# Performance work log

Measured on AMD Instinct MI355X. Metric: run time of the kernel, lower is better.

## Reference

```python
import jax, jax.numpy as jnp
import numpy as np

D_MODEL = 768
N_HEADS = 12
HEAD_DIM = D_MODEL // N_HEADS
B, T = 2, 2048


def setup_inputs() -> dict:
    key = jax.random.key(0)
    k1, k2, k3 = jax.random.split(key, 3)
    x = jax.random.normal(k1, (B, T, D_MODEL), dtype=jnp.float32)
    # causal mask: positions where mask == 0 (False) get -inf
    mask = jnp.tril(jnp.ones((T, T), dtype=bool))[None, None, :, :]
    Wqkv = jax.random.normal(k2, (D_MODEL, 3 * D_MODEL), dtype=jnp.float32) * (D_MODEL ** -0.5)
    bqkv = jnp.zeros((3 * D_MODEL,), dtype=jnp.float32)
    Wout = jax.random.normal(k3, (D_MODEL, D_MODEL), dtype=jnp.float32) * (D_MODEL ** -0.5)
    bout = jnp.zeros((D_MODEL,), dtype=jnp.float32)
    return {"x": x, "mask": mask, "Wqkv": Wqkv, "bqkv": bqkv, "Wout": Wout, "bout": bout}


def reference(x, mask, Wqkv, bqkv, Wout, bout):
    b, t, c = x.shape
    qkv = x @ Wqkv + bqkv                      # [B, T, 3C]
    q, k, v = jnp.split(qkv, 3, axis=-1)
    def heads(z):  # [B, T, C] -> [B, H, T, Dh]
        return z.reshape(b, t, N_HEADS, HEAD_DIM).transpose(0, 2, 1, 3)
    q, k, v = heads(q), heads(k), heads(v)
    scores = jnp.einsum('bhqd,bhkd->bhqk', q, k) / jnp.sqrt(jnp.float32(HEAD_DIM))
    scores = jnp.where(mask, scores, -jnp.inf)
    attn = jax.nn.softmax(scores, axis=-1)
    out = jnp.einsum('bhqk,bhkd->bhqd', attn, v)  # [B, H, T, Dh]
    out = out.transpose(0, 2, 1, 3).reshape(b, t, c)
    # dropout is identity in eval mode
    return out @ Wout + bout
```

## Files before the change

kernel.cpp:

```cpp
#include <hip/hip_runtime.h>
#include <math.h>

#define BB 2
#define TT 2048
#define CC 768
#define HH 12
#define DD 64
#define MROWS (BB*TT)
#define NQKV (3*CC)
#define QBLK 64

typedef short bf16x8 __attribute__((ext_vector_type(8)));
typedef float f32x4 __attribute__((ext_vector_type(4)));

__device__ __forceinline__ unsigned short f2bf(float f) {
    union { float f; unsigned u; } v; v.f = f;
    unsigned u = v.u + 0x7FFF + ((v.u >> 16) & 1);
    return (unsigned short)(u >> 16);
}

__device__ __forceinline__ unsigned cvtpk_bf16(float lo, float hi) {
    unsigned r;
    asm("v_cvt_pk_bf16_f32 %0, %1, %2" : "=v"(r) : "v"(lo), "v"(hi));
    return r;
}

__device__ __forceinline__ void gload_lds16(const void* g, void* l) {
    __builtin_amdgcn_global_load_lds(
        (const __attribute__((address_space(1))) unsigned int*)g,
        (__attribute__((address_space(3))) unsigned int*)l, 16, 0, 0);
}

#define XBLOCKS 512
#define TQKV_TILES ((NQKV/64)*(CC/64))
#define TOUT_TILES ((CC/64)*(CC/64))

__global__ __launch_bounds__(256) void prep(const float* __restrict__ x,
                                            const float* __restrict__ Wqkv,
                                            const float* __restrict__ Wout,
                                            unsigned short* __restrict__ xb,
                                            unsigned short* __restrict__ wqkv_t,
                                            unsigned short* __restrict__ wout_t)
{
    int bid = blockIdx.x;
    if (bid < XBLOCKS) {
        const int total8 = MROWS * CC / 8;
        for (int i = bid * 256 + threadIdx.x; i < total8; i += XBLOCKS * 256) {
            float4 a = ((const float4*)x)[i * 2];
            float4 b = ((const float4*)x)[i * 2 + 1];
            ushort4 lo = { f2bf(a.x), f2bf(a.y), f2bf(a.z), f2bf(a.w) };
            ushort4 hi = { f2bf(b.x), f2bf(b.y), f2bf(b.z), f2bf(b.w) };
            ((ushort4*)xb)[i * 2]     = lo;
            ((ushort4*)xb)[i * 2 + 1] = hi;
        }
        return;
    }
    bid -= XBLOCKS;
    const float* src; unsigned short* dst; int srcN, nt, kt;
    if (bid < TQKV_TILES) { src = Wqkv; dst = wqkv_t; srcN = NQKV;
                            nt = bid % (NQKV/64); kt = bid / (NQKV/64); }
    else { bid -= TQKV_TILES; src = Wout; dst = wout_t; srcN = CC;
           nt = bid % (CC/64); kt = bid / (CC/64); }

    __shared__ float Ts[64][65];
    const int n0 = nt * 64, k0 = kt * 64;
#pragma unroll
    for (int p = 0; p < 4; ++p) {
        int c = p * 256 + threadIdx.x;
        int row = c >> 4, col4 = c & 15;
        float4 v = *(const float4*)&src[(size_t)(k0 + row) * srcN + n0 + col4 * 4];
        Ts[row][col4 * 4 + 0] = v.x;
        Ts[row][col4 * 4 + 1] = v.y;
        Ts[row][col4 * 4 + 2] = v.z;
        Ts[row][col4 * 4 + 3] = v.w;
    }
    __syncthreads();
#pragma unroll
    for (int p = 0; p < 4; ++p) {
        int t = p * 256 + threadIdx.x;
        int on = t >> 4, oslot = t & 15;
        ushort4 o = { f2bf(Ts[oslot * 4 + 0][on]), f2bf(Ts[oslot * 4 + 1][on]),
                      f2bf(Ts[oslot * 4 + 2][on]), f2bf(Ts[oslot * 4 + 3][on]) };
        *(ushort4*)&dst[(size_t)(n0 + on) * CC + k0 + oslot * 4] = o;
    }
}

__global__ __launch_bounds__(256) void qkv_mfma(const unsigned short* __restrict__ A,
                                                const unsigned short* __restrict__ Bt,
                                                const float* __restrict__ bias,
                                                unsigned short* __restrict__ qb,
                                                unsigned short* __restrict__ kb,
                                                unsigned short* __restrict__ vb)
{
    __shared__ unsigned short As[64 * 64];
    __shared__ unsigned short Bs[128 * 64];
    const int tid = threadIdx.x;
    const int wv = tid >> 6, l = tid & 63, g = l >> 4, lr = l & 15;
    const int wm = wv >> 1, wn = wv & 1;
    const int m0 = blockIdx.y * 64, n0 = blockIdx.x * 128;
    const int h7 = lr & 7;

    f32x4 acc[2][4] = {};

    for (int k0 = 0; k0 < CC; k0 += 64) {
        __syncthreads();
#pragma unroll
        for (int p = 0; p < 2; ++p) {
            int c = p * 256 + tid;
            int row = c >> 3, slot = c & 7;
            int ss = slot ^ (row & 7);
            gload_lds16(A + (size_t)(m0 + row) * CC + k0 + ss * 8, As + c * 8);
        }
#pragma unroll
        for (int p = 0; p < 4; ++p) {
            int c = p * 256 + tid;
            int row = c >> 3, slot = c & 7;
            int ss = slot ^ (row & 7);
            gload_lds16(Bt + (size_t)(n0 + row) * CC + k0 + ss * 8, Bs + c * 8);
        }
        __syncthreads();
        bf16x8 af[2][2], bfr[4][2];
#pragma unroll
        for (int i = 0; i < 2; ++i)
#pragma unroll
            for (int kt = 0; kt < 2; ++kt) {
                int row = wm * 32 + i * 16 + lr;
                af[i][kt] = *(const bf16x8*)&As[row * 64 + ((kt * 4 + g) ^ h7) * 8];
            }
#pragma unroll
        for (int j = 0; j < 4; ++j)
#pragma unroll
            for (int kt = 0; kt < 2; ++kt) {
                int row = wn * 64 + j * 16 + lr;
                bfr[j][kt] = *(const bf16x8*)&Bs[row * 64 + ((kt * 4 + g) ^ h7) * 8];
            }
#pragma unroll
        for (int i = 0; i < 2; ++i)
#pragma unroll
            for (int j = 0; j < 4; ++j)
#pragma unroll
                for (int kt = 0; kt < 2; ++kt)
                    acc[i][j] = __builtin_amdgcn_mfma_f32_16x16x32_bf16(af[i][kt], bfr[j][kt], acc[i][j], 0, 0, 0);
    }

#pragma unroll
    for (int i = 0; i < 2; ++i)
#pragma unroll
        for (int r = 0; r < 4; ++r) {
            int m = m0 + wm * 32 + i * 16 + 4 * g + r;
            int b_ = m >> 11, t = m & (TT - 1);
#pragma unroll
            for (int j = 0; j < 4; ++j) {
                int n = n0 + wn * 64 + j * 16 + lr;
                float val = acc[i][j][r] + bias[n];
                int which = n / CC;
                int rr = n - which * CC;
                int h = rr >> 6, d = rr & 63;
                size_t bh = (size_t)b_ * HH + h;
                if (which == 0)      qb[(bh * TT + t) * DD + d] = f2bf(val * 0.18033688f);
                else if (which == 1) kb[(bh * TT + t) * DD + d] = f2bf(val);
                else                 vb[(bh * DD + d) * TT + t] = f2bf(val);
            }
        }
}

__global__ __launch_bounds__(256) void out_mfma(const unsigned short* __restrict__ A,
                                                const unsigned short* __restrict__ Bt,
                                                const float* __restrict__ bias,
                                                float* __restrict__ out)
{
    __shared__ unsigned short As[64 * 64];
    __shared__ unsigned short Bs[128 * 64];
    const int tid = threadIdx.x;
    const int wv = tid >> 6, l = tid & 63, g = l >> 4, lr = l & 15;
    const int wm = wv >> 1, wn = wv & 1;
    const int m0 = blockIdx.y * 64, n0 = blockIdx.x * 128;
    const int h7 = lr & 7;

    f32x4 acc[2][4] = {};

    for (int k0 = 0; k0 < CC; k0 += 64) {
        __syncthreads();
#pragma unroll
        for (int p = 0; p < 2; ++p) {
            int c = p * 256 + tid;
            int row = c >> 3, slot = c & 7;
            int ss = slot ^ (row & 7);
            gload_lds16(A + (size_t)(m0 + row) * CC + k0 + ss * 8, As + c * 8);
        }
#pragma unroll
        for (int p = 0; p < 4; ++p) {
            int c = p * 256 + tid;
            int row = c >> 3, slot = c & 7;
            int ss = slot ^ (row & 7);
            gload_lds16(Bt + (size_t)(n0 + row) * CC + k0 + ss * 8, Bs + c * 8);
        }
        __syncthreads();
        bf16x8 af[2][2], bfr[4][2];
#pragma unroll
        for (int i = 0; i < 2; ++i)
#pragma unroll
            for (int kt = 0; kt < 2; ++kt) {
                int row = wm * 32 + i * 16 + lr;
                af[i][kt] = *(const bf16x8*)&As[row * 64 + ((kt * 4 + g) ^ h7) * 8];
            }
#pragma unroll
        for (int j = 0; j < 4; ++j)
#pragma unroll
            for (int kt = 0; kt < 2; ++kt) {
                int row = wn * 64 + j * 16 + lr;
                bfr[j][kt] = *(const bf16x8*)&Bs[row * 64 + ((kt * 4 + g) ^ h7) * 8];
            }
#pragma unroll
        for (int i = 0; i < 2; ++i)
#pragma unroll
            for (int j = 0; j < 4; ++j)
#pragma unroll
                for (int kt = 0; kt < 2; ++kt)
                    acc[i][j] = __builtin_amdgcn_mfma_f32_16x16x32_bf16(af[i][kt], bfr[j][kt], acc[i][j], 0, 0, 0);
    }

#pragma unroll
    for (int i = 0; i < 2; ++i)
#pragma unroll
        for (int r = 0; r < 4; ++r) {
            int m = m0 + wm * 32 + i * 16 + 4 * g + r;
#pragma unroll
            for (int j = 0; j < 4; ++j) {
                int n = n0 + wn * 64 + j * 16 + lr;
                out[(size_t)m * CC + n] = acc[i][j][r] + bias[n];
            }
        }
}

__global__ __launch_bounds__(256) void attn_mfma(
    const unsigned short* __restrict__ qb,
    const unsigned short* __restrict__ kb,
    const unsigned short* __restrict__ vtb,
    unsigned short* __restrict__ outp)
{
    __shared__ unsigned short Ks[2 * 64 * 64];
    __shared__ unsigned short Vts[2 * 64 * 64];

    const int blk  = blockIdx.x;
    const int head = blk % (BB * HH);
    const int qt   = (TT / QBLK - 1) - blk / (BB * HH);
    const int tid  = threadIdx.x;
    const int wv   = tid >> 6;
    const int l    = tid & 63;
    const int g    = l >> 4;
    const int lr   = l & 15;

    const size_t hb = (size_t)head * TT * DD;
    const int qrow0 = qt * QBLK + wv * 16;

    bf16x8 qf[2];
#pragma unroll
    for (int dt = 0; dt < 2; ++dt)
        qf[dt] = *(const bf16x8*)(qb + hb + (size_t)(qrow0 + lr) * DD + dt * 32 + 8 * g);

    f32x4 oacc[4] = {};
    float lpart = 0.f;

    const int srow0 = tid >> 3, srow1 = srow0 + 32;
    const int slot  = tid & 7;
#define RHO(k) ((((k) >> 5) << 5) | ((((k) >> 2) & 1) << 4) | ((((k) >> 3) & 3) << 2) | ((k) & 3))
    const int rho0 = RHO(srow0), rho1 = RHO(srow1);
    const int koff0 = (rho0 * 64 + slot * 8) ^ ((rho0 & 7) << 3);
    const int koff1 = (rho1 * 64 + slot * 8) ^ ((rho1 & 7) << 3);
    const int voff0 = (srow0 * 64 + slot * 8) ^ ((srow0 & 7) << 3);
    const int voff1 = (srow1 * 64 + slot * 8) ^ ((srow1 & 7) << 3);
    const unsigned short* kg0 = kb  + hb + (size_t)srow0 * DD + slot * 8;
    const unsigned short* kg1 = kb  + hb + (size_t)srow1 * DD + slot * 8;
    const unsigned short* vg0 = vtb + hb + (size_t)srow0 * TT + slot * 8;
    const unsigned short* vg1 = vtb + hb + (size_t)srow1 * TT + slot * 8;

    *(bf16x8*)&Ks[koff0]  = *(const bf16x8*)(kg0);
    *(bf16x8*)&Ks[koff1]  = *(const bf16x8*)(kg1);
    *(bf16x8*)&Vts[voff0] = *(const bf16x8*)(vg0);
    *(bf16x8*)&Vts[voff1] = *(const bf16x8*)(vg1);
    __syncthreads();

    int bo = 0;
    for (int c = 0; c <= qt; ++c) {
        const bool more = (c < qt);
        bf16x8 nk0, nk1, nv0, nv1;
        if (more) {
            nk0 = *(const bf16x8*)(kg0 + (size_t)(c + 1) * 64 * DD);
            nk1 = *(const bf16x8*)(kg1 + (size_t)(c + 1) * 64 * DD);
            nv0 = *(const bf16x8*)(vg0 + (c + 1) * 64);
            nv1 = *(const bf16x8*)(vg1 + (c + 1) * 64);
        }

        f32x4 sacc[4] = {};
        __builtin_amdgcn_s_setprio(1);
#pragma unroll
        for (int jt = 0; jt < 4; ++jt) {
#pragma unroll
            for (int dt = 0; dt < 2; ++dt) {
                int prow = jt * 16 + lr;
                int off = bo + ((prow * 64 + dt * 32 + g * 8) ^ ((prow & 7) << 3));
                bf16x8 kf = *(const bf16x8*)&Ks[off];
                sacc[jt] = __builtin_amdgcn_mfma_f32_16x16x32_bf16(kf, qf[dt], sacc[jt], 0, 0, 0);
            }
        }
        __builtin_amdgcn_s_setprio(0);

        float pv[4][4];
        const int qloc = wv * 16 + lr;
        const bool diag = (c == qt);
#pragma unroll
        for (int jt = 0; jt < 4; ++jt)
#pragma unroll
            for (int r = 0; r < 4; ++r) {
                float p = __builtin_amdgcn_exp2f(sacc[jt][r]);
                if (diag) {
                    int keyl = 32 * (jt >> 1) + 8 * g + 4 * (jt & 1) + r;
                    if (keyl > qloc) p = 0.f;
                }
                pv[jt][r] = p;
                lpart += p;
            }

        union { bf16x8 v; unsigned u[4]; } pf0, pf1;
        pf0.u[0] = cvtpk_bf16(pv[0][0], pv[0][1]);
        pf0.u[1] = cvtpk_bf16(pv[0][2], pv[0][3]);
        pf0.u[2] = cvtpk_bf16(pv[1][0], pv[1][1]);
        pf0.u[3] = cvtpk_bf16(pv[1][2], pv[1][3]);
        pf1.u[0] = cvtpk_bf16(pv[2][0], pv[2][1]);
        pf1.u[1] = cvtpk_bf16(pv[2][2], pv[2][3]);
        pf1.u[2] = cvtpk_bf16(pv[3][0], pv[3][1]);
        pf1.u[3] = cvtpk_bf16(pv[3][2], pv[3][3]);

        __builtin_amdgcn_s_setprio(1);
#pragma unroll
        for (int dt = 0; dt < 4; ++dt) {
#pragma unroll
            for (int kt = 0; kt < 2; ++kt) {
                int row = dt * 16 + lr;
                int off = bo + ((row * 64 + kt * 32 + g * 8) ^ ((row & 7) << 3));
                bf16x8 vf = *(const bf16x8*)&Vts[off];
                oacc[dt] = __builtin_amdgcn_mfma_f32_16x16x32_bf16(
                    kt ? pf1.v : pf0.v, vf, oacc[dt], 0, 0, 0);
            }
        }
        __builtin_amdgcn_s_setprio(0);

        if (more) {
            int nb = bo ^ (64 * 64);
            *(bf16x8*)&Ks[nb + koff0]  = nk0;
            *(bf16x8*)&Ks[nb + koff1]  = nk1;
            *(bf16x8*)&Vts[nb + voff0] = nv0;
            *(bf16x8*)&Vts[nb + voff1] = nv1;
            __syncthreads();
            bo = nb;
        }
    }

    float lsum = lpart;
    lsum += __shfl_xor(lsum, 16);
    lsum += __shfl_xor(lsum, 32);
    float linv[4];
#pragma unroll
    for (int r = 0; r < 4; ++r)
        linv[r] = 1.f / __shfl(lsum, 4 * g + r);

    const int b_ = head / HH, h = head % HH;
#pragma unroll
    for (int dt = 0; dt < 4; ++dt)
#pragma unroll
        for (int r = 0; r < 4; ++r) {
            int qg = qrow0 + 4 * g + r;
            outp[((size_t)b_ * TT + qg) * CC + h * DD + dt * 16 + lr] =
                f2bf(oacc[dt][r] * linv[r]);
        }
}

extern "C" void kernel_launch(void* const* d_in, const int* in_sizes, int n_in,
                              void* d_out, int out_size, void* d_ws, size_t ws_size,
                              hipStream_t stream)
{
    const float* x    = (const float*)d_in[0];
    const float* Wqkv = (const float*)d_in[2];
    const float* bqkv = (const float*)d_in[3];
    const float* Wout = (const float*)d_in[4];
    const float* bout = (const float*)d_in[5];
    float* out = (float*)d_out;

    unsigned short* p = (unsigned short*)d_ws;
    unsigned short* xb      = p;  p += (size_t)MROWS * CC;
    unsigned short* wqkv_t  = p;  p += (size_t)NQKV * CC;
    unsigned short* wout_t  = p;  p += (size_t)CC * CC;
    unsigned short* qb      = p;  p += (size_t)BB * HH * TT * DD;
    unsigned short* kb      = p;  p += (size_t)BB * HH * TT * DD;
    unsigned short* vb      = p;  p += (size_t)BB * HH * TT * DD;
    unsigned short* attnb   = p;  p += (size_t)MROWS * CC;

    prep<<<XBLOCKS + TQKV_TILES + TOUT_TILES, 256, 0, stream>>>(x, Wqkv, Wout, xb, wqkv_t, wout_t);

    dim3 g1(NQKV / 128, MROWS / 64);
    qkv_mfma<<<g1, 256, 0, stream>>>(xb, wqkv_t, bqkv, qb, kb, vb);

    dim3 g2(BB * HH * (TT / QBLK));
    attn_mfma<<<g2, 256, 0, stream>>>(qb, kb, vb, attnb);

    dim3 g3(CC / 128, MROWS / 64);
    out_mfma<<<g3, 256, 0, stream>>>(attnb, wout_t, bout, out);
}
```

Measured before the change: 171.1 us.

## Double-buffer LDS tiles in QKV and output projection GEMMs

Both projection GEMM kernels now hold two LDS buffers for the A and B tiles. The loads for the next K-step are issued before the MFMA work on the current buffer, and the two barriers per iteration become one. The aim is to hide global-to-LDS load latency behind the matrix math. In exchange, LDS use per block doubles, which can lower occupancy. The attention kernel is left unchanged and likely dominates total time.

```diff
diff --git a/kernel.cpp b/kernel.cpp
--- a/kernel.cpp
+++ b/kernel.cpp
@@ -9,6 +9,7 @@
 #define MROWS (BB*TT)
 #define NQKV (3*CC)
 #define QBLK 64
+#define NKSTEP (CC/64)
 
 typedef short bf16x8 __attribute__((ext_vector_type(8)));
 typedef float f32x4 __attribute__((ext_vector_type(4)));
@@ -92,8 +93,8 @@
                                                 unsigned short* __restrict__ kb,
                                                 unsigned short* __restrict__ vb)
 {
-    __shared__ unsigned short As[64 * 64];
-    __shared__ unsigned short Bs[128 * 64];
+    __shared__ unsigned short As[2 * 64 * 64];
+    __shared__ unsigned short Bs[2 * 128 * 64];
     const int tid = threadIdx.x;
     const int wv = tid >> 6, l = tid & 63, g = l >> 4, lr = l & 15;
     const int wm = wv >> 1, wn = wv & 1;
@@ -102,37 +103,49 @@
 
     f32x4 acc[2][4] = {};
 
-    for (int k0 = 0; k0 < CC; k0 += 64) {
-        __syncthreads();
+    const int cA  = tid;
+    auto stage = [&](int b, int k0) {
 #pragma unroll
         for (int p = 0; p < 2; ++p) {
             int c = p * 256 + tid;
             int row = c >> 3, slot = c & 7;
             int ss = slot ^ (row & 7);
-            gload_lds16(A + (size_t)(m0 + row) * CC + k0 + ss * 8, As + c * 8);
+            gload_lds16(A + (size_t)(m0 + row) * CC + k0 + ss * 8,
+                        As + b * (64 * 64) + c * 8);
         }
 #pragma unroll
         for (int p = 0; p < 4; ++p) {
             int c = p * 256 + tid;
             int row = c >> 3, slot = c & 7;
             int ss = slot ^ (row & 7);
-            gload_lds16(Bt + (size_t)(n0 + row) * CC + k0 + ss * 8, Bs + c * 8);
-        }
-        __syncthreads();
+            gload_lds16(Bt + (size_t)(n0 + row) * CC + k0 + ss * 8,
+                        Bs + b * (128 * 64) + c * 8);
+        }
+    };
+    (void)cA;
+
+    stage(0, 0);
+    __syncthreads();
+
+    int buf = 0;
+    for (int ks = 0; ks < NKSTEP; ++ks) {
+        if (ks + 1 < NKSTEP) stage(buf ^ 1, (ks + 1) * 64);
+
+        const int ab = buf * (64 * 64), bb = buf * (128 * 64);
         bf16x8 af[2][2], bfr[4][2];
 #pragma unroll
         for (int i = 0; i < 2; ++i)
 #pragma unroll
             for (int kt = 0; kt < 2; ++kt) {
                 int row = wm * 32 + i * 16 + lr;
-                af[i][kt] = *(const bf16x8*)&As[row * 64 + ((kt * 4 + g) ^ h7) * 8];
+                af[i][kt] = *(const bf16x8*)&As[ab + row * 64 + ((kt * 4 + g) ^ h7) * 8];
             }
 #pragma unroll
         for (int j = 0; j < 4; ++j)
 #pragma unroll
             for (int kt = 0; kt < 2; ++kt) {
                 int row = wn * 64 + j * 16 + lr;
-                bfr[j][kt] = *(const bf16x8*)&Bs[row * 64 + ((kt * 4 + g) ^ h7) * 8];
+                bfr[j][kt] = *(const bf16x8*)&Bs[bb + row * 64 + ((kt * 4 + g) ^ h7) * 8];
             }
 #pragma unroll
         for (int i = 0; i < 2; ++i)
@@ -141,6 +154,9 @@
 #pragma unroll
                 for (int kt = 0; kt < 2; ++kt)
                     acc[i][j] = __builtin_amdgcn_mfma_f32_16x16x32_bf16(af[i][kt], bfr[j][kt], acc[i][j], 0, 0, 0);
+
+        __syncthreads();
+        buf ^= 1;
     }
 
 #pragma unroll
@@ -169,8 +185,8 @@
                                                 const float* __restrict__ bias,
                                                 float* __restrict__ out)
 {
-    __shared__ unsigned short As[64 * 64];
-    __shared__ unsigned short Bs[128 * 64];
+    __shared__ unsigned short As[2 * 64 * 64];
+    __shared__ unsigned short Bs[2 * 128 * 64];
     const int tid = threadIdx.x;
     const int wv = tid >> 6, l = tid & 63, g = l >> 4, lr = l & 15;
     const int wm = wv >> 1, wn = wv & 1;
@@ -179,37 +195,47 @@
 
     f32x4 acc[2][4] = {};
 
-    for (int k0 = 0; k0 < CC; k0 += 64) {
-        __syncthreads();
+    auto stage = [&](int b, int k0) {
 #pragma unroll
         for (int p = 0; p < 2; ++p) {
             int c = p * 256 + tid;
             int row = c >> 3, slot = c & 7;
             int ss = slot ^ (row & 7);
-            gload_lds16(A + (size_t)(m0 + row) * CC + k0 + ss * 8, As + c * 8);
+            gload_lds16(A + (size_t)(m0 + row) * CC + k0 + ss * 8,
+                        As + b * (64 * 64) + c * 8);
         }
 #pragma unroll
         for (int p = 0; p < 4; ++p) {
             int c = p * 256 + tid;
             int row = c >> 3, slot = c & 7;
             int ss = slot ^ (row & 7);
-            gload_lds16(Bt + (size_t)(n0 + row) * CC + k0 + ss * 8, Bs + c * 8);
-        }
-        __syncthreads();
+            gload_lds16(Bt + (size_t)(n0 + row) * CC + k0 + ss * 8,
+                        Bs + b * (128 * 64) + c * 8);
+        }
+    };
+
+    stage(0, 0);
+    __syncthreads();
+
+    int buf = 0;
+    for (int ks = 0; ks < NKSTEP; ++ks) {
+        if (ks + 1 < NKSTEP) stage(buf ^ 1, (ks + 1) * 64);
+
+        const int ab = buf * (64 * 64), bb = buf * (128 * 64);
         bf16x8 af[2][2], bfr[4][2];
 #pragma unroll
         for (int i = 0; i < 2; ++i)
 #pragma unroll
             for (int kt = 0; kt < 2; ++kt) {
                 int row = wm * 32 + i * 16 + lr;
-                af[i][kt] = *(const bf16x8*)&As[row * 64 + ((kt * 4 + g) ^ h7) * 8];
+                af[i][kt] = *(const bf16x8*)&As[ab + row * 64 + ((kt * 4 + g) ^ h7) * 8];
             }
 #pragma unroll
         for (int j = 0; j < 4; ++j)
 #pragma unroll
             for (int kt = 0; kt < 2; ++kt) {
                 int row = wn * 64 + j * 16 + lr;
-                bfr[j][kt] = *(const bf16x8*)&Bs[row * 64 + ((kt * 4 + g) ^ h7) * 8];
+                bfr[j][kt] = *(const bf16x8*)&Bs[bb + row * 64 + ((kt * 4 + g) ^ h7) * 8];
             }
 #pragma unroll
         for (int i = 0; i < 2; ++i)
@@ -218,6 +244,9 @@
 #pragma unroll
                 for (int kt = 0; kt < 2; ++kt)
                     acc[i][j] = __builtin_amdgcn_mfma_f32_16x16x32_bf16(af[i][kt], bfr[j][kt], acc[i][j], 0, 0, 0);
+
+        __syncthreads();
+        buf ^= 1;
     }
 
 #pragma unroll
```

Result: no change. 174.0 us (+1.7%).

## Fuse x fp32-to-bf16 conversion into QKV GEMM and shrink out-proj tile

Applied to the files above, without the earlier changes.

Removes the separate pass that converts x to bf16 in the prep kernel. The QKV GEMM now loads fp32 x directly, converts it in registers with packed cvt instructions, and writes the result to LDS. This saves a full read-write round trip of the activation but makes the A-tile load synchronous through registers instead of asynchronous global-to-LDS. The output projection tile also shrinks from 64x128 to 64x64, doubling the block count to improve occupancy on many CUs.

```diff
diff --git a/kernel.cpp b/kernel.cpp
--- a/kernel.cpp
+++ b/kernel.cpp
@@ -9,6 +9,7 @@
 #define MROWS (BB*TT)
 #define NQKV (3*CC)
 #define QBLK 64
+#define NKSTEP (CC/64)
 
 typedef short bf16x8 __attribute__((ext_vector_type(8)));
 typedef float f32x4 __attribute__((ext_vector_type(4)));
@@ -31,31 +32,15 @@
         (__attribute__((address_space(3))) unsigned int*)l, 16, 0, 0);
 }
 
-#define XBLOCKS 512
 #define TQKV_TILES ((NQKV/64)*(CC/64))
 #define TOUT_TILES ((CC/64)*(CC/64))
 
-__global__ __launch_bounds__(256) void prep(const float* __restrict__ x,
-                                            const float* __restrict__ Wqkv,
+__global__ __launch_bounds__(256) void prep(const float* __restrict__ Wqkv,
                                             const float* __restrict__ Wout,
-                                            unsigned short* __restrict__ xb,
                                             unsigned short* __restrict__ wqkv_t,
                                             unsigned short* __restrict__ wout_t)
 {
     int bid = blockIdx.x;
-    if (bid < XBLOCKS) {
-        const int total8 = MROWS * CC / 8;
-        for (int i = bid * 256 + threadIdx.x; i < total8; i += XBLOCKS * 256) {
-            float4 a = ((const float4*)x)[i * 2];
-            float4 b = ((const float4*)x)[i * 2 + 1];
-            ushort4 lo = { f2bf(a.x), f2bf(a.y), f2bf(a.z), f2bf(a.w) };
-            ushort4 hi = { f2bf(b.x), f2bf(b.y), f2bf(b.z), f2bf(b.w) };
-            ((ushort4*)xb)[i * 2]     = lo;
-            ((ushort4*)xb)[i * 2 + 1] = hi;
-        }
-        return;
-    }
-    bid -= XBLOCKS;
     const float* src; unsigned short* dst; int srcN, nt, kt;
     if (bid < TQKV_TILES) { src = Wqkv; dst = wqkv_t; srcN = NQKV;
                             nt = bid % (NQKV/64); kt = bid / (NQKV/64); }
@@ -85,7 +70,7 @@
     }
 }
 
-__global__ __launch_bounds__(256) void qkv_mfma(const unsigned short* __restrict__ A,
+__global__ __launch_bounds__(256) void qkv_mfma(const float* __restrict__ X,
                                                 const unsigned short* __restrict__ Bt,
                                                 const float* __restrict__ bias,
                                                 unsigned short* __restrict__ qb,
@@ -105,20 +90,29 @@
     for (int k0 = 0; k0 < CC; k0 += 64) {
         __syncthreads();
 #pragma unroll
-        for (int p = 0; p < 2; ++p) {
-            int c = p * 256 + tid;
-            int row = c >> 3, slot = c & 7;
-            int ss = slot ^ (row & 7);
-            gload_lds16(A + (size_t)(m0 + row) * CC + k0 + ss * 8, As + c * 8);
-        }
-#pragma unroll
         for (int p = 0; p < 4; ++p) {
             int c = p * 256 + tid;
             int row = c >> 3, slot = c & 7;
             int ss = slot ^ (row & 7);
             gload_lds16(Bt + (size_t)(n0 + row) * CC + k0 + ss * 8, Bs + c * 8);
         }
+#pragma unroll
+        for (int p = 0; p < 2; ++p) {
+            int c = p * 256 + tid;
+            int row = c >> 3, slot = c & 7;
+            int ss = slot ^ (row & 7);
+            const float* src = X + (size_t)(m0 + row) * CC + k0 + ss * 8;
+            float4 a0 = *(const float4*)src;
+            float4 a1 = *(const float4*)(src + 4);
+            union { bf16x8 v; unsigned u[4]; } w;
+            w.u[0] = cvtpk_bf16(a0.x, a0.y);
+            w.u[1] = cvtpk_bf16(a0.z, a0.w);
+            w.u[2] = cvtpk_bf16(a1.x, a1.y);
+            w.u[3] = cvtpk_bf16(a1.z, a1.w);
+            *(bf16x8*)&As[c * 8] = w.v;
+        }
         __syncthreads();
+
         bf16x8 af[2][2], bfr[4][2];
 #pragma unroll
         for (int i = 0; i < 2; ++i)
@@ -170,14 +164,14 @@
                                                 float* __restrict__ out)
 {
     __shared__ unsigned short As[64 * 64];
-    __shared__ unsigned short Bs[128 * 64];
+    __shared__ unsigned short Bs[64 * 64];
     const int tid = threadIdx.x;
     const int wv = tid >> 6, l = tid & 63, g = l >> 4, lr = l & 15;
     const int wm = wv >> 1, wn = wv & 1;
-    const int m0 = blockIdx.y * 64, n0 = blockIdx.x * 128;
+    const int m0 = blockIdx.y * 64, n0 = blockIdx.x * 64;
     const int h7 = lr & 7;
 
-    f32x4 acc[2][4] = {};
+    f32x4 acc[2][2] = {};
 
     for (int k0 = 0; k0 < CC; k0 += 64) {
         __syncthreads();
@@ -186,35 +180,24 @@
             int c = p * 256 + tid;
             int row = c >> 3, slot = c & 7;
             int ss = slot ^ (row & 7);
-            gload_lds16(A + (size_t)(m0 + row) * CC + k0 + ss * 8, As + c * 8);
-        }
-#pragma unroll
-        for (int p = 0; p < 4; ++p) {
-            int c = p * 256 + tid;
-            int row = c >> 3, slot = c & 7;
-            int ss = slot ^ (row & 7);
+            gload_lds16(A  + (size_t)(m0 + row) * CC + k0 + ss * 8, As + c * 8);
             gload_lds16(Bt + (size_t)(n0 + row) * CC + k0 + ss * 8, Bs + c * 8);
         }
         __syncthreads();
-        bf16x8 af[2][2], bfr[4][2];
+        bf16x8 af[2][2], bfr[2][2];
 #pragma unroll
         for (int i = 0; i < 2; ++i)
 #pragma unroll
             for (int kt = 0; kt < 2; ++kt) {
-                int row = wm * 32 + i * 16 + lr;
-                af[i][kt] = *(const bf16x8*)&As[row * 64 + ((kt * 4 + g) ^ h7) * 8];
-            }
-#pragma unroll
-        for (int j = 0; j < 4; ++j)
-#pragma unroll
-            for (int kt = 0; kt < 2; ++kt) {
-                int row = wn * 64 + j * 16 + lr;
-                bfr[j][kt] = *(const bf16x8*)&Bs[row * 64 + ((kt * 4 + g) ^ h7) * 8];
+                int arow = wm * 32 + i * 16 + lr;
+                af[i][kt] = *(const bf16x8*)&As[arow * 64 + ((kt * 4 + g) ^ h7) * 8];
+                int brow = wn * 32 + i * 16 + lr;
+                bfr[i][kt] = *(const bf16x8*)&Bs[brow * 64 + ((kt * 4 + g) ^ h7) * 8];
             }
 #pragma unroll
         for (int i = 0; i < 2; ++i)
 #pragma unroll
-            for (int j = 0; j < 4; ++j)
+            for (int j = 0; j < 2; ++j)
 #pragma unroll
                 for (int kt = 0; kt < 2; ++kt)
                     acc[i][j] = __builtin_amdgcn_mfma_f32_16x16x32_bf16(af[i][kt], bfr[j][kt], acc[i][j], 0, 0, 0);
@@ -226,8 +209,8 @@
         for (int r = 0; r < 4; ++r) {
             int m = m0 + wm * 32 + i * 16 + 4 * g + r;
 #pragma unroll
-            for (int j = 0; j < 4; ++j) {
-                int n = n0 + wn * 64 + j * 16 + lr;
+            for (int j = 0; j < 2; ++j) {
+                int n = n0 + wn * 32 + j * 16 + lr;
                 out[(size_t)m * CC + n] = acc[i][j][r] + bias[n];
             }
         }
@@ -388,7 +371,6 @@
     float* out = (float*)d_out;
 
     unsigned short* p = (unsigned short*)d_ws;
-    unsigned short* xb      = p;  p += (size_t)MROWS * CC;
     unsigned short* wqkv_t  = p;  p += (size_t)NQKV * CC;
     unsigned short* wout_t  = p;  p += (size_t)CC * CC;
     unsigned short* qb      = p;  p += (size_t)BB * HH * TT * DD;
@@ -396,14 +378,14 @@
     unsigned short* vb      = p;  p += (size_t)BB * HH * TT * DD;
     unsigned short* attnb   = p;  p += (size_t)MROWS * CC;
 
-    prep<<<XBLOCKS + TQKV_TILES + TOUT_TILES, 256, 0, stream>>>(x, Wqkv, Wout, xb, wqkv_t, wout_t);
+    prep<<<TQKV_TILES + TOUT_TILES, 256, 0, stream>>>(Wqkv, Wout, wqkv_t, wout_t);
 
     dim3 g1(NQKV / 128, MROWS / 64);
-    qkv_mfma<<<g1, 256, 0, stream>>>(xb, wqkv_t, bqkv, qb, kb, vb);
+    qkv_mfma<<<g1, 256, 0, stream>>>(x, wqkv_t, bqkv, qb, kb, vb);
 
     dim3 g2(BB * HH * (TT / QBLK));
     attn_mfma<<<g2, 256, 0, stream>>>(qb, kb, vb, attnb);
 
-    dim3 g3(CC / 128, MROWS / 64);
+    dim3 g3(CC / 64, MROWS / 64);
     out_mfma<<<g3, 256, 0, stream>>>(attnb, wout_t, bout, out);
 }
```

Measured after the change: 174.5 us. Within noise of the previous version (+2.0%).
